# Kernel optimization log

Hardware: AMD Instinct MI355X
Metric: run time of the kernel (lower is better)

The kernel has to match this reference:

```python
import jax, jax.numpy as jnp
import numpy as np

B, T, D = 16, 1024, 512      # batch, query time, model hidden
C = 4096                     # context entries
DC = 512                     # context hidden
A = 512                      # attndim
P = 512                      # proj hidden


def setup_inputs() -> dict:
    key = jax.random.key(0)
    ks = jax.random.split(key, 10)
    s = lambda fan_in: 1.0 / np.sqrt(fan_in)
    return {
        "model_embed": jax.random.normal(ks[0], (B, T, D), jnp.float32),
        "context_embed": jax.random.normal(ks[1], (C, DC), jnp.float32),
        "Wq": jax.random.uniform(ks[2], (D, A), jnp.float32, -s(D), s(D)),
        "bq": jax.random.uniform(ks[3], (A,), jnp.float32, -s(D), s(D)),
        "Wk": jax.random.uniform(ks[4], (DC, A), jnp.float32, -s(DC), s(DC)),
        "bk": jax.random.uniform(ks[5], (A,), jnp.float32, -s(DC), s(DC)),
        "Wv": jax.random.uniform(ks[6], (DC, A), jnp.float32, -s(DC), s(DC)),
        "bv": jax.random.uniform(ks[7], (A,), jnp.float32, -s(DC), s(DC)),
        "Wo": jax.random.uniform(ks[8], (A, P), jnp.float32, -s(A), s(A)),
        "bo": jax.random.uniform(ks[9], (P,), jnp.float32, -s(A), s(A)),
    }


def reference(model_embed, context_embed, Wq, bq, Wk, bk, Wv, bv, Wo, bo):
    q = model_embed @ Wq + bq            # [B, T, A]
    k = context_embed @ Wk + bk          # [C, A]
    v = context_embed @ Wv + bv          # [C, A]
    scale = 1.0 / jnp.sqrt(jnp.asarray(q.shape[-1], q.dtype))
    scores = jnp.einsum('ck,btk->btc', k, q) * scale   # [B, T, C]
    attn = jax.nn.softmax(scores, axis=-1)             # softmax over context
    x = jnp.einsum('ck,btc->btk', v, attn)             # [B, T, A]
    return x @ Wo + bo                                 # [B, T, P]
```

## Files before the change

kernel.cpp:

```cpp
#include <hip/hip_runtime.h>

#define MB_T 16384
#define DD   512
#define CC   4096
#define AA   512
#define PP   512

typedef __attribute__((ext_vector_type(4))) float f32x4;
typedef __attribute__((ext_vector_type(8))) short short8;

#define MFMA16(a, b, c) __builtin_amdgcn_mfma_f32_16x16x32_bf16((a), (b), (c), 0, 0, 0)

__device__ __forceinline__ unsigned short f2bf(float f) {
  union { float f; unsigned int u; } cv; cv.f = f;
  unsigned int u = cv.u;
  return (unsigned short)((u + 0x7FFFu + ((u >> 16) & 1u)) >> 16);
}
__device__ __forceinline__ float bf2f(unsigned short u) {
  union { unsigned int i; float f; } c; c.i = (unsigned int)u << 16; return c.f;
}

__device__ __forceinline__ void gload16(const unsigned short* g, unsigned short* l) {
  __builtin_amdgcn_global_load_lds(
      (const __attribute__((address_space(1))) unsigned int*)g,
      (__attribute__((address_space(3))) unsigned int*)l, 16, 0, 0);
}

__global__ void cast_bf16_kernel(const float* __restrict__ in,
                                 unsigned short* __restrict__ out, int n4) {
  int i = blockIdx.x * blockDim.x + threadIdx.x;
  int stride = gridDim.x * blockDim.x;
  for (; i < n4; i += stride) {
    float4 v = reinterpret_cast<const float4*>(in)[i];
    ushort4 o;
    o.x = f2bf(v.x); o.y = f2bf(v.y); o.z = f2bf(v.z); o.w = f2bf(v.w);
    reinterpret_cast<ushort4*>(out)[i] = o;
  }
}

__global__ void cast3_kernel(const float* __restrict__ i0, const float* __restrict__ i1,
                             const float* __restrict__ i2, unsigned short* __restrict__ o0,
                             unsigned short* __restrict__ o1, unsigned short* __restrict__ o2,
                             int n4) {
  const float* in = blockIdx.y == 0 ? i0 : blockIdx.y == 1 ? i1 : i2;
  unsigned short* out = blockIdx.y == 0 ? o0 : blockIdx.y == 1 ? o1 : o2;
  int i = blockIdx.x * blockDim.x + threadIdx.x;
  if (i < n4) {
    float4 v = reinterpret_cast<const float4*>(in)[i];
    ushort4 o;
    o.x = f2bf(v.x); o.y = f2bf(v.y); o.z = f2bf(v.z); o.w = f2bf(v.w);
    reinterpret_cast<ushort4*>(out)[i] = o;
  }
}

__global__ __launch_bounds__(256) void transpose_cast_kernel(
    const float* __restrict__ W, unsigned short* __restrict__ WT, int rows, int cols) {
  __shared__ float t_s[32][33];
  int bi = blockIdx.y * 32, bj = blockIdx.x * 32;
  int r = threadIdx.x >> 3, c4 = (threadIdx.x & 7) * 4;
  float4 v = *reinterpret_cast<const float4*>(W + (size_t)(bi + r) * cols + bj + c4);
  t_s[r][c4 + 0] = v.x; t_s[r][c4 + 1] = v.y;
  t_s[r][c4 + 2] = v.z; t_s[r][c4 + 3] = v.w;
  __syncthreads();
  ushort4 o;
  o.x = f2bf(t_s[c4 + 0][r]);
  o.y = f2bf(t_s[c4 + 1][r]);
  o.z = f2bf(t_s[c4 + 2][r]);
  o.w = f2bf(t_s[c4 + 3][r]);
  *reinterpret_cast<ushort4*>(WT + (size_t)(bj + r) * rows + bi + c4) = o;
}

__device__ __forceinline__ void rowdot_body(const unsigned short* mat, const float* vec,
                                            float* outv, float scale) {
  const int lane = threadIdx.x & 63, wid = threadIdx.x >> 6;
  const int row = blockIdx.x * 4 + wid;
  const unsigned short* kr = mat + (size_t)row * 512 + lane * 8;
  float s = 0.f;
  ushort4 a = *reinterpret_cast<const ushort4*>(kr);
  ushort4 b = *reinterpret_cast<const ushort4*>(kr + 4);
  const float* bqp = vec + lane * 8;
  s += bf2f(a.x) * bqp[0]; s += bf2f(a.y) * bqp[1];
  s += bf2f(a.z) * bqp[2]; s += bf2f(a.w) * bqp[3];
  s += bf2f(b.x) * bqp[4]; s += bf2f(b.y) * bqp[5];
  s += bf2f(b.z) * bqp[6]; s += bf2f(b.w) * bqp[7];
#pragma unroll
  for (int d = 1; d < 64; d <<= 1) s += __shfl_xor(s, d);
  if (lane == 0) outv[row] = s * scale;
}

__global__ __launch_bounds__(256) void rowdot_kernel(
    const unsigned short* __restrict__ mat, const float* __restrict__ vec,
    float* __restrict__ outv, float scale) {
  rowdot_body(mat, vec, outv, scale);
}

__global__ __launch_bounds__(256) void rowdot3_kernel(
    const unsigned short* m0, const float* v0, float* o0, float s0,
    const unsigned short* m1, const float* v1, float* o1, float s1,
    const unsigned short* m2, const float* v2, float* o2, float s2) {
  if (blockIdx.y == 0) rowdot_body(m0, v0, o0, s0);
  else if (blockIdx.y == 1) rowdot_body(m1, v1, o1, s1);
  else rowdot_body(m2, v2, o2, s2);
}

__global__ __launch_bounds__(256) void reduce_lsum_kernel(
    const float* __restrict__ lsp, float* __restrict__ lsum) {
  int m = blockIdx.x * blockDim.x + threadIdx.x;
  const float4* p = reinterpret_cast<const float4*>(lsp + (size_t)m * 64);
  float s = 0.f;
#pragma unroll
  for (int j = 0; j < 16; ++j) { float4 v = p[j]; s += v.x + v.y + v.z + v.w; }
  lsum[m] = s;
}

template <int MODE, int TM, int OCC>
__global__ __launch_bounds__(256, OCC) void gemm2p_kernel(
    const unsigned short* __restrict__ A, const unsigned short* __restrict__ BT,
    const float* __restrict__ bias, const float* __restrict__ rowsum_in,
    void* __restrict__ Cout, int M, int N, int K, float alpha) {
  constexpr int MFR = TM / 32;
  constexpr int WROW = TM / 2;
  constexpr int ASZ = TM * 32;
  constexpr int BSZ = 128 * 32;
  __shared__ unsigned short lds[2 * ASZ + 2 * BSZ];

  const int tid = threadIdx.x;
  const int lane = tid & 63, wid = tid >> 6;
  const int hq = lane >> 4, lq = lane & 15;
  const int wm = wid >> 1, wn = wid & 1;

  const int gx = gridDim.x;
  const int nwg = gx * gridDim.y;
  const int orig = blockIdx.y * gx + blockIdx.x;
  const int swz = (orig & 7) * (nwg >> 3) + (orig >> 3);
  const int bx = swz % gx, by = swz / gx;
  const int brow = by * TM, bcol = bx * 128;

  const unsigned short* ap = A + (size_t)(brow + (tid >> 2)) * K + (tid & 3) * 8;
  const unsigned short* bp = BT + (size_t)(bcol + (tid >> 2)) * K + (tid & 3) * 8;
  const size_t row64 = (size_t)64 * K;

  const int nt = K >> 5;
#pragma unroll
  for (int j = 0; j < TM / 64; ++j)
    gload16(ap + j * row64, lds + wid * 512 + j * 2048);
  gload16(bp, lds + 2 * ASZ + wid * 512);
  gload16(bp + row64, lds + 2 * ASZ + wid * 512 + 2048);
  __syncthreads();

  f32x4 acc[MFR][4] = {};
  for (int t = 0; t < nt; ++t) {
    const int cur = t & 1;
    if (t + 1 < nt) {
      const int k0 = (t + 1) * 32;
      unsigned short* an = lds + (cur ^ 1) * ASZ + wid * 512;
      unsigned short* bn = lds + 2 * ASZ + (cur ^ 1) * BSZ + wid * 512;
#pragma unroll
      for (int j = 0; j < TM / 64; ++j)
        gload16(ap + k0 + j * row64, an + j * 2048);
      gload16(bp + k0, bn);
      gload16(bp + k0 + row64, bn + 2048);
    }
    const unsigned short* as0 = lds + cur * ASZ;
    const unsigned short* bs0 = lds + 2 * ASZ + cur * BSZ;
    short8 af[MFR], bfv[4];
#pragma unroll
    for (int mf = 0; mf < MFR; ++mf)
      af[mf] = *reinterpret_cast<const short8*>(&as0[(wm * WROW + mf * 16 + lq) * 32 + hq * 8]);
#pragma unroll
    for (int nf = 0; nf < 4; ++nf)
      bfv[nf] = *reinterpret_cast<const short8*>(&bs0[(wn * 64 + nf * 16 + lq) * 32 + hq * 8]);
#pragma unroll
    for (int mf = 0; mf < MFR; ++mf)
#pragma unroll
      for (int nf = 0; nf < 4; ++nf)
        acc[mf][nf] = MFMA16(af[mf], bfv[nf], acc[mf][nf]);
    if (t + 1 < nt) __syncthreads();
  }

  if (MODE == 5) {
#pragma unroll
    for (int mf = 0; mf < MFR; ++mf)
#pragma unroll
      for (int i = 0; i < 4; ++i) {
        const int rowg = brow + wm * WROW + mf * 16 + hq * 4 + i;
        const float inv = 1.0f / rowsum_in[rowg];
#pragma unroll
        for (int nf = 0; nf < 4; ++nf) {
          const int colg = bcol + wn * 64 + nf * 16 + lq;
          ((float*)Cout)[(size_t)rowg * N + colg] = acc[mf][nf][i] * inv + bias[colg];
        }
      }
  } else if (MODE == 1) {
#pragma unroll
    for (int nf = 0; nf < 4; ++nf) {
      const int colg = bcol + wn * 64 + nf * 16 + lq;
      const float bv = bias ? bias[colg] : 0.f;
#pragma unroll
      for (int mf = 0; mf < MFR; ++mf) {
        const int rowg0 = brow + wm * WROW + mf * 16 + hq * 4;
        ushort4 pk;
        pk.x = f2bf(acc[mf][nf][0] + bv);
        pk.y = f2bf(acc[mf][nf][1] + bv);
        pk.z = f2bf(acc[mf][nf][2] + bv);
        pk.w = f2bf(acc[mf][nf][3] + bv);
        *reinterpret_cast<ushort4*>((unsigned short*)Cout + (size_t)colg * M + rowg0) = pk;
      }
    }
  } else {
#pragma unroll
    for (int nf = 0; nf < 4; ++nf) {
      const int colg = bcol + wn * 64 + nf * 16 + lq;
      const float bv = bias ? bias[colg] : 0.f;
#pragma unroll
      for (int mf = 0; mf < MFR; ++mf) {
        const int rowg0 = brow + wm * WROW + mf * 16 + hq * 4;
#pragma unroll
        for (int i = 0; i < 4; ++i)
          ((unsigned short*)Cout)[(size_t)(rowg0 + i) * N + colg] =
              f2bf((acc[mf][nf][i] + bv) * alpha);
      }
    }
  }
}

__global__ __launch_bounds__(256, 3) void gemm3b_kernel(
    const unsigned short* __restrict__ A, const unsigned short* __restrict__ BT,
    const float* __restrict__ colbias, float* __restrict__ psum_out,
    unsigned short* __restrict__ Cout, int M, int N, int K) {
  __shared__ unsigned short lds[3 * 8192];
  const int tid = threadIdx.x;
  const int lane = tid & 63, wid = tid >> 6;
  const int hq = lane >> 4, lq = lane & 15;
  const int wm = wid >> 1, wn = wid & 1;

  const int gx = gridDim.x;
  const int nwg = gx * gridDim.y;
  const int orig = blockIdx.y * gx + blockIdx.x;
  const int swz = (orig & 7) * (nwg >> 3) + (orig >> 3);
  const int bx = swz % gx, by = swz / gx;
  const int brow = by * 128, bcol = bx * 128;

  const unsigned short* ap = A + (size_t)(brow + (tid >> 2)) * K + (tid & 3) * 8;
  const unsigned short* bp = BT + (size_t)(bcol + (tid >> 2)) * K + (tid & 3) * 8;
  const size_t row64 = (size_t)64 * K;
  const int dst = wid * 512;

  const int nt = K >> 5;
#pragma unroll
  for (int tt = 0; tt < 2; ++tt) {
    unsigned short* ab = lds + tt * 8192;
    gload16(ap + tt * 32, ab + dst);
    gload16(ap + tt * 32 + row64, ab + dst + 2048);
    gload16(bp + tt * 32, ab + 4096 + dst);
    gload16(bp + tt * 32 + row64, ab + 4096 + dst + 2048);
  }
  asm volatile("s_waitcnt vmcnt(4)" ::: "memory");
  __builtin_amdgcn_s_barrier();

  f32x4 acc[4][4] = {};
  for (int t = 0; t < nt; ++t) {
    const unsigned short* ab = lds + (t % 3) * 8192;
    if (t + 2 < nt) {
      const int k0 = (t + 2) * 32;
      unsigned short* nb = lds + ((t + 2) % 3) * 8192;
      gload16(ap + k0, nb + dst);
      gload16(ap + k0 + row64, nb + dst + 2048);
      gload16(bp + k0, nb + 4096 + dst);
      gload16(bp + k0 + row64, nb + 4096 + dst + 2048);
    }
    short8 af[4], bfv[4];
#pragma unroll
    for (int mf = 0; mf < 4; ++mf)
      af[mf] = *reinterpret_cast<const short8*>(&ab[(wm * 64 + mf * 16 + lq) * 32 + hq * 8]);
#pragma unroll
    for (int nf = 0; nf < 4; ++nf)
      bfv[nf] = *reinterpret_cast<const short8*>(&ab[4096 + (wn * 64 + nf * 16 + lq) * 32 + hq * 8]);
    __builtin_amdgcn_s_setprio(1);
#pragma unroll
    for (int mf = 0; mf < 4; ++mf)
#pragma unroll
      for (int nf = 0; nf < 4; ++nf)
        acc[mf][nf] = MFMA16(af[mf], bfv[nf], acc[mf][nf]);
    __builtin_amdgcn_s_setprio(0);
    if (t + 2 < nt) {
      asm volatile("s_waitcnt vmcnt(4)" ::: "memory");
      __builtin_amdgcn_s_barrier();
    } else if (t + 1 < nt) {
      asm volatile("s_waitcnt vmcnt(0)" ::: "memory");
      __builtin_amdgcn_s_barrier();
    }
  }

  float cb[4];
#pragma unroll
  for (int nf = 0; nf < 4; ++nf) cb[nf] = colbias[bcol + wn * 64 + nf * 16 + lq];
#pragma unroll
  for (int p = 0; p < 2; ++p) {
    __syncthreads();
    if (wm == p) {
#pragma unroll
      for (int mf = 0; mf < 4; ++mf)
#pragma unroll
        for (int i = 0; i < 4; ++i) {
          const int rl = mf * 16 + hq * 4 + i;
          float s = 0.f;
#pragma unroll
          for (int nf = 0; nf < 4; ++nf) {
            float pv = __expf(acc[mf][nf][i] + cb[nf]);
            s += pv;
            lds[rl * 136 + wn * 64 + nf * 16 + lq] = f2bf(pv);
          }
          s += __shfl_xor(s, 1);
          s += __shfl_xor(s, 2);
          s += __shfl_xor(s, 4);
          s += __shfl_xor(s, 8);
          if (lq == 0) psum_out[(size_t)(brow + p * 64 + rl) * 64 + bx * 2 + wn] = s;
        }
    }
    __syncthreads();
#pragma unroll
    for (int j = 0; j < 4; ++j) {
      const int chunk = j * 256 + tid;
      const int row = chunk >> 4, c = chunk & 15;
      short8 v = *reinterpret_cast<const short8*>(&lds[row * 136 + c * 8]);
      *reinterpret_cast<short8*>(Cout + (size_t)(brow + p * 64 + row) * N + bcol + c * 8) = v;
    }
  }
}

extern "C" void kernel_launch(void* const* d_in, const int* in_sizes, int n_in,
                              void* d_out, int out_size, void* d_ws, size_t ws_size,
                              hipStream_t stream) {
  const float* model = (const float*)d_in[0];
  const float* ctx   = (const float*)d_in[1];
  const float* Wq = (const float*)d_in[2]; const float* bq = (const float*)d_in[3];
  const float* Wk = (const float*)d_in[4]; const float* bk = (const float*)d_in[5];
  const float* Wv = (const float*)d_in[6]; const float* bv = (const float*)d_in[7];
  const float* Wo = (const float*)d_in[8]; const float* bo = (const float*)d_in[9];
  float* out = (float*)d_out;

  char* ws = (char*)d_ws;
  size_t off = 0;
  auto alloc = [&](size_t bytes) -> void* {
    void* p = ws + off;
    off += (bytes + 255) & ~(size_t)255;
    return p;
  };
  unsigned short* model_bf = (unsigned short*)alloc((size_t)MB_T * DD * 2);
  unsigned short* ctx_bf   = (unsigned short*)alloc((size_t)CC * DD * 2);
  unsigned short* Wq_bf = (unsigned short*)alloc((size_t)DD * AA * 2);
  unsigned short* Wk_bf = (unsigned short*)alloc((size_t)DD * AA * 2);
  unsigned short* Wv_bf = (unsigned short*)alloc((size_t)DD * AA * 2);
  unsigned short* WoT   = (unsigned short*)alloc((size_t)AA * PP * 2);
  unsigned short* WkqT_bf = (unsigned short*)alloc((size_t)DD * DD * 2);
  unsigned short* WvoT_bf = (unsigned short*)alloc((size_t)PP * DD * 2);
  unsigned short* KqT_bf  = (unsigned short*)alloc((size_t)CC * DD * 2);
  unsigned short* W2T_bf  = (unsigned short*)alloc((size_t)PP * CC * 2);
  float* bkq  = (float*)alloc((size_t)DD * 4);
  float* bvo  = (float*)alloc((size_t)PP * 4);
  float* wkbq = (float*)alloc((size_t)DD * 4);
  float* bqk  = (float*)alloc((size_t)CC * 4);
  float* lsp  = (float*)alloc((size_t)MB_T * 64 * 4);
  float* lsum = (float*)alloc((size_t)MB_T * 4);
  unsigned short* P_bf = (unsigned short*)alloc((size_t)MB_T * CC * 2);

  const float scale = 0.04419417382415922f;

  cast_bf16_kernel<<<2048, 256, 0, stream>>>(model, model_bf, MB_T * DD / 4);
  cast_bf16_kernel<<<1024, 256, 0, stream>>>(ctx, ctx_bf, CC * DD / 4);
  cast3_kernel<<<dim3(256, 3), 256, 0, stream>>>(Wq, Wk, Wv, Wq_bf, Wk_bf, Wv_bf,
                                                 DD * AA / 4);
  transpose_cast_kernel<<<dim3(16, 16), 256, 0, stream>>>(Wo, WoT, AA, PP);

  rowdot3_kernel<<<dim3(128, 3), 256, 0, stream>>>(
      Wq_bf, bk, bkq, scale,
      Wk_bf, bq, wkbq, scale,
      WoT, bv, bvo, 1.0f);
  rowdot_kernel<<<CC / 4, 256, 0, stream>>>(ctx_bf, wkbq, bqk, 1.0f);

  gemm2p_kernel<0, 128, 4><<<dim3(4, 4), 256, 0, stream>>>(
      Wq_bf, Wk_bf, nullptr, nullptr, WkqT_bf, DD, DD, AA, scale);
  gemm2p_kernel<0, 128, 4><<<dim3(4, 4), 256, 0, stream>>>(
      WoT, Wv_bf, nullptr, nullptr, WvoT_bf, PP, DD, AA, 1.0f);

  gemm2p_kernel<0, 128, 4><<<dim3(4, 32), 256, 0, stream>>>(
      ctx_bf, WkqT_bf, bkq, nullptr, KqT_bf, CC, DD, DD, 1.0f);
  gemm2p_kernel<1, 128, 4><<<dim3(4, 32), 256, 0, stream>>>(
      ctx_bf, WvoT_bf, bvo, nullptr, W2T_bf, CC, PP, DD, 1.0f);

  gemm3b_kernel<<<dim3(32, 128), 256, 0, stream>>>(
      model_bf, KqT_bf, bqk, lsp, P_bf, MB_T, CC, DD);

  reduce_lsum_kernel<<<MB_T / 256, 256, 0, stream>>>(lsp, lsum);

  gemm2p_kernel<5, 64, 5><<<dim3(4, 256), 256, 0, stream>>>(
      P_bf, W2T_bf, bo, lsum, out, MB_T, PP, CC, 1.0f);
}
```

Measured before the change: 369.4 us.

## Use 8-wave 256-wide tiles with 4-stage LDS pipeline for scores and output GEMMs

Replaces the 128x128 scores GEMM and the 64x128 output GEMM with 512-thread kernels using 256x256 and 256x128 tiles. Both use a 4-deep global_load_lds ring with XOR-swizzled LDS chunks to cut bank conflicts. The scores kernel splits its A loads and MFMAs into two halves per k-step so loads interleave with compute. Bigger tiles mean more reuse per byte loaded, but occupancy drops to one workgroup per CU and the grid shrinks (256 blocks for the output GEMM), which may underfill the device.

```diff
diff --git a/kernel.cpp b/kernel.cpp
--- a/kernel.cpp
+++ b/kernel.cpp
@@ -113,17 +113,12 @@
   lsum[m] = s;
 }
 
-template <int MODE, int TM, int OCC>
-__global__ __launch_bounds__(256, OCC) void gemm2p_kernel(
+template <int MODE>
+__global__ __launch_bounds__(256, 4) void gemm2p_kernel(
     const unsigned short* __restrict__ A, const unsigned short* __restrict__ BT,
-    const float* __restrict__ bias, const float* __restrict__ rowsum_in,
-    void* __restrict__ Cout, int M, int N, int K, float alpha) {
-  constexpr int MFR = TM / 32;
-  constexpr int WROW = TM / 2;
-  constexpr int ASZ = TM * 32;
-  constexpr int BSZ = 128 * 32;
-  __shared__ unsigned short lds[2 * ASZ + 2 * BSZ];
-
+    const float* __restrict__ bias, void* __restrict__ Cout,
+    int M, int N, int K, float alpha) {
+  __shared__ unsigned short lds[4 * 4096];
   const int tid = threadIdx.x;
   const int lane = tid & 63, wid = tid >> 6;
   const int hq = lane >> 4, lq = lane & 15;
@@ -134,71 +129,56 @@
   const int orig = blockIdx.y * gx + blockIdx.x;
   const int swz = (orig & 7) * (nwg >> 3) + (orig >> 3);
   const int bx = swz % gx, by = swz / gx;
-  const int brow = by * TM, bcol = bx * 128;
+  const int brow = by * 128, bcol = bx * 128;
 
   const unsigned short* ap = A + (size_t)(brow + (tid >> 2)) * K + (tid & 3) * 8;
   const unsigned short* bp = BT + (size_t)(bcol + (tid >> 2)) * K + (tid & 3) * 8;
   const size_t row64 = (size_t)64 * K;
 
   const int nt = K >> 5;
-#pragma unroll
-  for (int j = 0; j < TM / 64; ++j)
-    gload16(ap + j * row64, lds + wid * 512 + j * 2048);
-  gload16(bp, lds + 2 * ASZ + wid * 512);
-  gload16(bp + row64, lds + 2 * ASZ + wid * 512 + 2048);
+  gload16(ap, lds + wid * 512);
+  gload16(ap + row64, lds + wid * 512 + 2048);
+  gload16(bp, lds + 8192 + wid * 512);
+  gload16(bp + row64, lds + 8192 + wid * 512 + 2048);
   __syncthreads();
 
-  f32x4 acc[MFR][4] = {};
+  f32x4 acc[4][4] = {};
   for (int t = 0; t < nt; ++t) {
     const int cur = t & 1;
     if (t + 1 < nt) {
       const int k0 = (t + 1) * 32;
-      unsigned short* an = lds + (cur ^ 1) * ASZ + wid * 512;
-      unsigned short* bn = lds + 2 * ASZ + (cur ^ 1) * BSZ + wid * 512;
-#pragma unroll
-      for (int j = 0; j < TM / 64; ++j)
-        gload16(ap + k0 + j * row64, an + j * 2048);
+      unsigned short* an = lds + (cur ^ 1) * 4096 + wid * 512;
+      unsigned short* bn = lds + 8192 + (cur ^ 1) * 4096 + wid * 512;
+      gload16(ap + k0, an);
+      gload16(ap + k0 + row64, an + 2048);
       gload16(bp + k0, bn);
       gload16(bp + k0 + row64, bn + 2048);
     }
-    const unsigned short* as0 = lds + cur * ASZ;
-    const unsigned short* bs0 = lds + 2 * ASZ + cur * BSZ;
-    short8 af[MFR], bfv[4];
-#pragma unroll
-    for (int mf = 0; mf < MFR; ++mf)
-      af[mf] = *reinterpret_cast<const short8*>(&as0[(wm * WROW + mf * 16 + lq) * 32 + hq * 8]);
+    const unsigned short* as0 = lds + cur * 4096;
+    const unsigned short* bs0 = lds + 8192 + cur * 4096;
+    short8 af[4], bfv[4];
+#pragma unroll
+    for (int mf = 0; mf < 4; ++mf)
+      af[mf] = *reinterpret_cast<const short8*>(&as0[(wm * 64 + mf * 16 + lq) * 32 + hq * 8]);
 #pragma unroll
     for (int nf = 0; nf < 4; ++nf)
       bfv[nf] = *reinterpret_cast<const short8*>(&bs0[(wn * 64 + nf * 16 + lq) * 32 + hq * 8]);
 #pragma unroll
-    for (int mf = 0; mf < MFR; ++mf)
+    for (int mf = 0; mf < 4; ++mf)
 #pragma unroll
       for (int nf = 0; nf < 4; ++nf)
         acc[mf][nf] = MFMA16(af[mf], bfv[nf], acc[mf][nf]);
     if (t + 1 < nt) __syncthreads();
   }
 
-  if (MODE == 5) {
-#pragma unroll
-    for (int mf = 0; mf < MFR; ++mf)
-#pragma unroll
-      for (int i = 0; i < 4; ++i) {
-        const int rowg = brow + wm * WROW + mf * 16 + hq * 4 + i;
-        const float inv = 1.0f / rowsum_in[rowg];
-#pragma unroll
-        for (int nf = 0; nf < 4; ++nf) {
-          const int colg = bcol + wn * 64 + nf * 16 + lq;
-          ((float*)Cout)[(size_t)rowg * N + colg] = acc[mf][nf][i] * inv + bias[colg];
-        }
-      }
-  } else if (MODE == 1) {
+  if (MODE == 1) {
 #pragma unroll
     for (int nf = 0; nf < 4; ++nf) {
       const int colg = bcol + wn * 64 + nf * 16 + lq;
       const float bv = bias ? bias[colg] : 0.f;
 #pragma unroll
-      for (int mf = 0; mf < MFR; ++mf) {
-        const int rowg0 = brow + wm * WROW + mf * 16 + hq * 4;
+      for (int mf = 0; mf < 4; ++mf) {
+        const int rowg0 = brow + wm * 64 + mf * 16 + hq * 4;
         ushort4 pk;
         pk.x = f2bf(acc[mf][nf][0] + bv);
         pk.y = f2bf(acc[mf][nf][1] + bv);
@@ -213,8 +193,8 @@
       const int colg = bcol + wn * 64 + nf * 16 + lq;
       const float bv = bias ? bias[colg] : 0.f;
 #pragma unroll
-      for (int mf = 0; mf < MFR; ++mf) {
-        const int rowg0 = brow + wm * WROW + mf * 16 + hq * 4;
+      for (int mf = 0; mf < 4; ++mf) {
+        const int rowg0 = brow + wm * 64 + mf * 16 + hq * 4;
 #pragma unroll
         for (int i = 0; i < 4; ++i)
           ((unsigned short*)Cout)[(size_t)(rowg0 + i) * N + colg] =
@@ -224,58 +204,60 @@
   }
 }
 
-__global__ __launch_bounds__(256, 3) void gemm3b_kernel(
+__global__ __launch_bounds__(512, 1) void gemm8p_scores_kernel(
     const unsigned short* __restrict__ A, const unsigned short* __restrict__ BT,
     const float* __restrict__ colbias, float* __restrict__ psum_out,
     unsigned short* __restrict__ Cout, int M, int N, int K) {
-  __shared__ unsigned short lds[3 * 8192];
+  __shared__ unsigned short lds[67584];
   const int tid = threadIdx.x;
   const int lane = tid & 63, wid = tid >> 6;
   const int hq = lane >> 4, lq = lane & 15;
-  const int wm = wid >> 1, wn = wid & 1;
+  const int wm = wid >> 2, wn = wid & 3;
 
   const int gx = gridDim.x;
   const int nwg = gx * gridDim.y;
   const int orig = blockIdx.y * gx + blockIdx.x;
   const int swz = (orig & 7) * (nwg >> 3) + (orig >> 3);
   const int bx = swz % gx, by = swz / gx;
-  const int brow = by * 128, bcol = bx * 128;
-
-  const unsigned short* ap = A + (size_t)(brow + (tid >> 2)) * K + (tid & 3) * 8;
-  const unsigned short* bp = BT + (size_t)(bcol + (tid >> 2)) * K + (tid & 3) * 8;
-  const size_t row64 = (size_t)64 * K;
+  const int brow = by * 256, bcol = bx * 256;
+
+  const int srow = tid >> 2;
+  const int schunk = (tid & 3) ^ ((tid >> 3) & 3);
+  const unsigned short* aS = A + (size_t)(brow + srow) * K + schunk * 8;
+  const unsigned short* bS = BT + (size_t)(bcol + srow) * K + schunk * 8;
+  const size_t row128 = (size_t)128 * K;
   const int dst = wid * 512;
 
   const int nt = K >> 5;
-#pragma unroll
-  for (int tt = 0; tt < 2; ++tt) {
-    unsigned short* ab = lds + tt * 8192;
-    gload16(ap + tt * 32, ab + dst);
-    gload16(ap + tt * 32 + row64, ab + dst + 2048);
-    gload16(bp + tt * 32, ab + 4096 + dst);
-    gload16(bp + tt * 32 + row64, ab + 4096 + dst + 2048);
-  }
-  asm volatile("s_waitcnt vmcnt(4)" ::: "memory");
+#define SSTAGE_A(tt) do { const int k0 = (tt) * 32;                         \
+    unsigned short* bb = lds + ((tt) & 3) * 16384;                          \
+    gload16(aS + k0, bb + dst); gload16(aS + row128 + k0, bb + 4096 + dst); } while (0)
+#define SSTAGE_B(tt) do { const int k0 = (tt) * 32;                         \
+    unsigned short* bb = lds + ((tt) & 3) * 16384 + 8192;                   \
+    gload16(bS + k0, bb + dst); gload16(bS + row128 + k0, bb + 4096 + dst); } while (0)
+
+  SSTAGE_A(0); SSTAGE_B(0);
+  SSTAGE_A(1); SSTAGE_B(1);
+  SSTAGE_A(2); SSTAGE_B(2);
+  asm volatile("s_waitcnt vmcnt(8)" ::: "memory");
   __builtin_amdgcn_s_barrier();
 
-  f32x4 acc[4][4] = {};
+  const int cswz = ((lq >> 1) & 3);
+  f32x4 acc[8][4] = {};
   for (int t = 0; t < nt; ++t) {
-    const unsigned short* ab = lds + (t % 3) * 8192;
-    if (t + 2 < nt) {
-      const int k0 = (t + 2) * 32;
-      unsigned short* nb = lds + ((t + 2) % 3) * 8192;
-      gload16(ap + k0, nb + dst);
-      gload16(ap + k0 + row64, nb + dst + 2048);
-      gload16(bp + k0, nb + 4096 + dst);
-      gload16(bp + k0 + row64, nb + 4096 + dst + 2048);
-    }
-    short8 af[4], bfv[4];
-#pragma unroll
-    for (int mf = 0; mf < 4; ++mf)
-      af[mf] = *reinterpret_cast<const short8*>(&ab[(wm * 64 + mf * 16 + lq) * 32 + hq * 8]);
+    const unsigned short* ab = lds + (t & 3) * 16384;
+    const unsigned short* bb = ab + 8192;
+    short8 bfv[4], af[4];
 #pragma unroll
     for (int nf = 0; nf < 4; ++nf)
-      bfv[nf] = *reinterpret_cast<const short8*>(&ab[4096 + (wn * 64 + nf * 16 + lq) * 32 + hq * 8]);
+      bfv[nf] = *reinterpret_cast<const short8*>(
+          &bb[(wn * 64 + nf * 16 + lq) * 32 + (hq ^ cswz) * 8]);
+#pragma unroll
+    for (int mf = 0; mf < 4; ++mf)
+      af[mf] = *reinterpret_cast<const short8*>(
+          &ab[(wm * 128 + mf * 16 + lq) * 32 + (hq ^ cswz) * 8]);
+    if (t + 3 < nt) SSTAGE_A(t + 3);
+    __builtin_amdgcn_s_barrier();
     __builtin_amdgcn_s_setprio(1);
 #pragma unroll
     for (int mf = 0; mf < 4; ++mf)
@@ -283,50 +265,135 @@
       for (int nf = 0; nf < 4; ++nf)
         acc[mf][nf] = MFMA16(af[mf], bfv[nf], acc[mf][nf]);
     __builtin_amdgcn_s_setprio(0);
-    if (t + 2 < nt) {
-      asm volatile("s_waitcnt vmcnt(4)" ::: "memory");
-      __builtin_amdgcn_s_barrier();
-    } else if (t + 1 < nt) {
-      asm volatile("s_waitcnt vmcnt(0)" ::: "memory");
-      __builtin_amdgcn_s_barrier();
+    __builtin_amdgcn_s_barrier();
+#pragma unroll
+    for (int mf = 0; mf < 4; ++mf)
+      af[mf] = *reinterpret_cast<const short8*>(
+          &ab[(wm * 128 + (mf + 4) * 16 + lq) * 32 + (hq ^ cswz) * 8]);
+    if (t + 3 < nt) SSTAGE_B(t + 3);
+    __builtin_amdgcn_s_barrier();
+    __builtin_amdgcn_s_setprio(1);
+#pragma unroll
+    for (int mf = 0; mf < 4; ++mf)
+#pragma unroll
+      for (int nf = 0; nf < 4; ++nf)
+        acc[mf + 4][nf] = MFMA16(af[mf], bfv[nf], acc[mf + 4][nf]);
+    __builtin_amdgcn_s_setprio(0);
+    if (t + 3 < nt)      asm volatile("s_waitcnt vmcnt(8)" ::: "memory");
+    else if (t + 2 < nt) asm volatile("s_waitcnt vmcnt(4)" ::: "memory");
+    else if (t + 1 < nt) asm volatile("s_waitcnt vmcnt(0)" ::: "memory");
+    __builtin_amdgcn_s_barrier();
+  }
+#undef SSTAGE_A
+#undef SSTAGE_B
+
+  float cb[4];
+#pragma unroll
+  for (int nf = 0; nf < 4; ++nf) cb[nf] = colbias[bcol + wn * 64 + nf * 16 + lq];
+#pragma unroll
+  for (int mf = 0; mf < 8; ++mf)
+#pragma unroll
+    for (int i = 0; i < 4; ++i) {
+      const int rowl = wm * 128 + mf * 16 + hq * 4 + i;
+      float s = 0.f;
+#pragma unroll
+      for (int nf = 0; nf < 4; ++nf) {
+        float pv = __expf(acc[mf][nf][i] + cb[nf]);
+        s += pv;
+        lds[rowl * 264 + wn * 64 + nf * 16 + lq] = f2bf(pv);
+      }
+      s += __shfl_xor(s, 1);
+      s += __shfl_xor(s, 2);
+      s += __shfl_xor(s, 4);
+      s += __shfl_xor(s, 8);
+      if (lq == 0) psum_out[(size_t)(brow + rowl) * 64 + bx * 4 + wn] = s;
     }
-  }
-
-  float cb[4];
-#pragma unroll
-  for (int nf = 0; nf < 4; ++nf) cb[nf] = colbias[bcol + wn * 64 + nf * 16 + lq];
-#pragma unroll
-  for (int p = 0; p < 2; ++p) {
-    __syncthreads();
-    if (wm == p) {
-#pragma unroll
-      for (int mf = 0; mf < 4; ++mf)
-#pragma unroll
-        for (int i = 0; i < 4; ++i) {
-          const int rl = mf * 16 + hq * 4 + i;
-          float s = 0.f;
-#pragma unroll
-          for (int nf = 0; nf < 4; ++nf) {
-            float pv = __expf(acc[mf][nf][i] + cb[nf]);
-            s += pv;
-            lds[rl * 136 + wn * 64 + nf * 16 + lq] = f2bf(pv);
-          }
-          s += __shfl_xor(s, 1);
-          s += __shfl_xor(s, 2);
-          s += __shfl_xor(s, 4);
-          s += __shfl_xor(s, 8);
-          if (lq == 0) psum_out[(size_t)(brow + p * 64 + rl) * 64 + bx * 2 + wn] = s;
-        }
+  __syncthreads();
+#pragma unroll
+  for (int j = 0; j < 16; ++j) {
+    const int c = j * 512 + tid;
+    const int row = c >> 5, ch = c & 31;
+    short8 v = *reinterpret_cast<const short8*>(&lds[row * 264 + ch * 8]);
+    *reinterpret_cast<short8*>(Cout + (size_t)(brow + row) * N + bcol + ch * 8) = v;
+  }
+}
+
+__global__ __launch_bounds__(512, 1) void gemm8p_out_kernel(
+    const unsigned short* __restrict__ A, const unsigned short* __restrict__ BT,
+    const float* __restrict__ bias, const float* __restrict__ rowsum_in,
+    float* __restrict__ Cout, int M, int N, int K) {
+  __shared__ unsigned short lds[4 * 12288];
+  const int tid = threadIdx.x;
+  const int lane = tid & 63, wid = tid >> 6;
+  const int hq = lane >> 4, lq = lane & 15;
+  const int wm = wid >> 1, wn = wid & 1;
+
+  const int gx = gridDim.x;
+  const int nwg = gx * gridDim.y;
+  const int orig = blockIdx.y * gx + blockIdx.x;
+  const int swz = (orig & 7) * (nwg >> 3) + (orig >> 3);
+  const int bx = swz % gx, by = swz / gx;
+  const int brow = by * 256, bcol = bx * 128;
+
+  const int srow = tid >> 2;
+  const int schunk = (tid & 3) ^ ((tid >> 3) & 3);
+  const unsigned short* aS = A + (size_t)(brow + srow) * K + schunk * 8;
+  const unsigned short* bS = BT + (size_t)(bcol + srow) * K + schunk * 8;
+  const size_t row128 = (size_t)128 * K;
+  const int dst = wid * 512;
+
+  const int nt = K >> 5;
+#define OSTAGE(tt) do { const int k0 = (tt) * 32;                            \
+    unsigned short* bb = lds + ((tt) & 3) * 12288;                           \
+    gload16(aS + k0, bb + dst); gload16(aS + row128 + k0, bb + 4096 + dst);  \
+    gload16(bS + k0, bb + 8192 + dst); } while (0)
+
+  OSTAGE(0); OSTAGE(1); OSTAGE(2);
+  asm volatile("s_waitcnt vmcnt(6)" ::: "memory");
+  __builtin_amdgcn_s_barrier();
+
+  const int cswz = ((lq >> 1) & 3);
+  f32x4 acc[4][4] = {};
+  for (int t = 0; t < nt; ++t) {
+    const unsigned short* ab = lds + (t & 3) * 12288;
+    const unsigned short* bb = ab + 8192;
+    short8 af[4], bfv[4];
+#pragma unroll
+    for (int mf = 0; mf < 4; ++mf)
+      af[mf] = *reinterpret_cast<const short8*>(
+          &ab[(wm * 64 + mf * 16 + lq) * 32 + (hq ^ cswz) * 8]);
+#pragma unroll
+    for (int nf = 0; nf < 4; ++nf)
+      bfv[nf] = *reinterpret_cast<const short8*>(
+          &bb[(wn * 64 + nf * 16 + lq) * 32 + (hq ^ cswz) * 8]);
+    if (t + 3 < nt) OSTAGE(t + 3);
+    __builtin_amdgcn_s_barrier();
+    __builtin_amdgcn_s_setprio(1);
+#pragma unroll
+    for (int mf = 0; mf < 4; ++mf)
+#pragma unroll
+      for (int nf = 0; nf < 4; ++nf)
+        acc[mf][nf] = MFMA16(af[mf], bfv[nf], acc[mf][nf]);
+    __builtin_amdgcn_s_setprio(0);
+    if (t + 3 < nt)      asm volatile("s_waitcnt vmcnt(6)" ::: "memory");
+    else if (t + 2 < nt) asm volatile("s_waitcnt vmcnt(3)" ::: "memory");
+    else if (t + 1 < nt) asm volatile("s_waitcnt vmcnt(0)" ::: "memory");
+    __builtin_amdgcn_s_barrier();
+  }
+#undef OSTAGE
+
+#pragma unroll
+  for (int mf = 0; mf < 4; ++mf)
+#pragma unroll
+    for (int i = 0; i < 4; ++i) {
+      const int rowg = brow + wm * 64 + mf * 16 + hq * 4 + i;
+      const float inv = 1.0f / rowsum_in[rowg];
+#pragma unroll
+      for (int nf = 0; nf < 4; ++nf) {
+        const int colg = bcol + wn * 64 + nf * 16 + lq;
+        Cout[(size_t)rowg * N + colg] = acc[mf][nf][i] * inv + bias[colg];
+      }
     }
-    __syncthreads();
-#pragma unroll
-    for (int j = 0; j < 4; ++j) {
-      const int chunk = j * 256 + tid;
-      const int row = chunk >> 4, c = chunk & 15;
-      short8 v = *reinterpret_cast<const short8*>(&lds[row * 136 + c * 8]);
-      *reinterpret_cast<short8*>(Cout + (size_t)(brow + p * 64 + row) * N + bcol + c * 8) = v;
-    }
-  }
 }
 
 extern "C" void kernel_launch(void* const* d_in, const int* in_sizes, int n_in,
@@ -379,21 +446,21 @@
       WoT, bv, bvo, 1.0f);
   rowdot_kernel<<<CC / 4, 256, 0, stream>>>(ctx_bf, wkbq, bqk, 1.0f);
 
-  gemm2p_kernel<0, 128, 4><<<dim3(4, 4), 256, 0, stream>>>(
-      Wq_bf, Wk_bf, nullptr, nullptr, WkqT_bf, DD, DD, AA, scale);
-  gemm2p_kernel<0, 128, 4><<<dim3(4, 4), 256, 0, stream>>>(
-      WoT, Wv_bf, nullptr, nullptr, WvoT_bf, PP, DD, AA, 1.0f);
-
-  gemm2p_kernel<0, 128, 4><<<dim3(4, 32), 256, 0, stream>>>(
-      ctx_bf, WkqT_bf, bkq, nullptr, KqT_bf, CC, DD, DD, 1.0f);
-  gemm2p_kernel<1, 128, 4><<<dim3(4, 32), 256, 0, stream>>>(
-      ctx_bf, WvoT_bf, bvo, nullptr, W2T_bf, CC, PP, DD, 1.0f);
-
-  gemm3b_kernel<<<dim3(32, 128), 256, 0, stream>>>(
+  gemm2p_kernel<0><<<dim3(4, 4), 256, 0, stream>>>(
+      Wq_bf, Wk_bf, nullptr, WkqT_bf, DD, DD, AA, scale);
+  gemm2p_kernel<0><<<dim3(4, 4), 256, 0, stream>>>(
+      WoT, Wv_bf, nullptr, WvoT_bf, PP, DD, AA, 1.0f);
+
+  gemm2p_kernel<0><<<dim3(4, 32), 256, 0, stream>>>(
+      ctx_bf, WkqT_bf, bkq, KqT_bf, CC, DD, DD, 1.0f);
+  gemm2p_kernel<1><<<dim3(4, 32), 256, 0, stream>>>(
+      ctx_bf, WvoT_bf, bvo, W2T_bf, CC, PP, DD, 1.0f);
+
+  gemm8p_scores_kernel<<<dim3(16, 64), 512, 0, stream>>>(
       model_bf, KqT_bf, bqk, lsp, P_bf, MB_T, CC, DD);
 
   reduce_lsum_kernel<<<MB_T / 256, 256, 0, stream>>>(lsp, lsum);
 
-  gemm2p_kernel<5, 64, 5><<<dim3(4, 256), 256, 0, stream>>>(
-      P_bf, W2T_bf, bo, lsum, out, MB_T, PP, CC, 1.0f);
-}
+  gemm8p_out_kernel<<<dim3(4, 64), 512, 0, stream>>>(
+      P_bf, W2T_bf, bo, lsum, out, MB_T, PP, CC);
+}
```

Result: faster. 336.4 us (-8.9%).
